# Kernel tuning notes

Hardware: AMD Instinct MI355X
Metric: run time of the kernel (lower is better)

Reference implementation:

```python
import jax, jax.numpy as jnp
import numpy as np

N_NODES = 8192
N_EDGES = 8192
DEG = 32          # nodes per hyperedge
NNZ = N_EDGES * DEG
D = 32            # embedding_dim / hidden_channels


def setup_inputs() -> dict:
    key = jax.random.key(0)
    ks = jax.random.split(key, 12)
    x_0 = jax.random.normal(ks[0], (N_NODES, D), dtype=jnp.float32)
    # incidence structure: each hyperedge touches DEG random nodes
    node_idx = jax.random.randint(ks[1], (NNZ,), 0, N_NODES)
    edge_idx = jnp.repeat(jnp.arange(N_EDGES), DEG)
    incidence_1 = jnp.zeros((N_NODES, N_EDGES), jnp.float32).at[node_idx, edge_idx].set(1.0)
    s = 1.0 / np.sqrt(D)
    # UniGCN layer weights (level-2 conv linear transform per layer, 2 layers)
    W_l1 = jax.random.uniform(ks[2], (D, D), jnp.float32, -s, s)
    W_l2 = jax.random.uniform(ks[3], (D, D), jnp.float32, -s, s)
    # 3-layer MLP (Linear(64,32), Linear(32,32), Linear(32,1)), no activations
    s2 = 1.0 / np.sqrt(2 * D)
    Wm1 = jax.random.uniform(ks[4], (2 * D, D), jnp.float32, -s2, s2)
    bm1 = jax.random.uniform(ks[5], (D,), jnp.float32, -s2, s2)
    Wm2 = jax.random.uniform(ks[6], (D, D), jnp.float32, -s, s)
    bm2 = jax.random.uniform(ks[7], (D,), jnp.float32, -s, s)
    Wm3 = jax.random.uniform(ks[8], (D, 1), jnp.float32, -s, s)
    bm3 = jax.random.uniform(ks[9], (1,), jnp.float32, -s, s)
    return {"x_0": x_0, "incidence_1": incidence_1,
            "W_l1": W_l1, "W_l2": W_l2,
            "Wm1": Wm1, "bm1": bm1, "Wm2": Wm2, "bm2": bm2,
            "Wm3": Wm3, "bm3": bm3,
            "node_idx": node_idx, "edge_idx": edge_idx}


def _unigcn(x_0, inc, W_l1, W_l2):
    # UniGCN layer: level1 (0->1, no linear transform), level2 (1->0, linear)
    x_1 = inc.T @ x_0                 # [E, D]
    x_0 = inc @ (x_1 @ W_l1)          # [N, D]
    x_1 = inc.T @ x_0                 # [E, D]
    x_0 = inc @ (x_1 @ W_l2)          # [N, D]
    return x_0, x_1


def reference(x_0, incidence_1, W_l1, W_l2, Wm1, bm1, Wm2, bm2, Wm3, bm3,
              node_idx, edge_idx):
    x_0_new, x_1_new = _unigcn(x_0, incidence_1, W_l1, W_l2)
    # gather embeddings at incidence nonzeros
    h = jnp.concatenate([x_0_new[node_idx], x_1_new[edge_idx]], axis=1)  # [NNZ, 2D]
    h = h @ Wm1 + bm1
    h = h @ Wm2 + bm2
    vals = (h @ Wm3 + bm3)[:, 0]                                          # [NNZ]
    # scatter back into dense [N, E] matrix
    output_counts = jnp.zeros_like(incidence_1).at[node_idx, edge_idx].set(vals)
    return output_counts
```

## Files before the change

### kernel.cpp

```cpp
#include <hip/hip_runtime.h>

#define N_NODES 8192
#define N_EDGES 8192
#define DEG 32
#define D 32
#define CAP 128

typedef float vf4 __attribute__((ext_vector_type(4)));


__global__ void __launch_bounds__(256)
k1_edge(const float* __restrict__ x0, const float* __restrict__ Wl1,
        const float* __restrict__ Wl2, const float* __restrict__ Wm1,
        const float* __restrict__ bm1, const float* __restrict__ Wm2,
        const float* __restrict__ bm2, const float* __restrict__ Wm3,
        const float* __restrict__ bm3, const int* __restrict__ node_idx,
        float* __restrict__ A, unsigned* __restrict__ validmask,
        int* __restrict__ cursor, int* __restrict__ csr_e,
        float* __restrict__ consts) {
    __shared__ int sidx[8][32];
    __shared__ unsigned smask[8];
    __shared__ float fsh[128];
    const int t = threadIdx.x, el = t >> 5, s = t & 31;

    if (blockIdx.x == 0) {
        float* w23 = fsh;
        float* M0  = fsh + 32;
        float* M1  = fsh + 64;
        float* w2u = fsh + 96;
        if (t < 32) {
            float acc = 0.f;
            for (int k = 0; k < 32; ++k) acc += Wm2[t * 32 + k] * Wm3[k];
            w23[t] = acc;
        }
        __syncthreads();
        if (t < 64) {
            float acc = 0.f;
            for (int k = 0; k < 32; ++k) acc += Wm1[t * 32 + k] * w23[k];
            if (t < 32) M0[t] = acc; else M1[t - 32] = acc;
        }
        if (t == 0) {
            float c = bm3[0];
            for (int k = 0; k < 32; ++k) c += bm1[k] * w23[k] + bm2[k] * Wm3[k];
            consts[0] = c;
        }
        __syncthreads();
        if (t < 32) {
            float acc = 0.f;
            for (int d2 = 0; d2 < 32; ++d2) acc += Wl2[t * 32 + d2] * M0[d2];
            w2u[t] = acc;
        }
        __syncthreads();
        if (t < 32) {
            float ay = 0.f, az = 0.f;
            for (int d2 = 0; d2 < 32; ++d2) {
                float w = Wl1[t * 32 + d2];
                ay += w * w2u[d2];
                az += w * M1[d2];
            }
            consts[1 + t]  = ay;
            consts[33 + t] = az;
        }
        __syncthreads();
    }

    int e = blockIdx.x * 8 + el;
    int idx = node_idx[e * DEG + s];
    sidx[el][s] = idx;
    __syncthreads();
    bool valid = true;
    for (int j = 0; j < s; ++j)
        if (sidx[el][j] == idx) { valid = false; break; }
    unsigned long long bl = __ballot(valid);
    if (s == 0) {
        unsigned m = (unsigned)(bl >> (t & 32));
        smask[el] = m;
        validmask[e] = m;
    }
    if (valid) {
        int pos = atomicAdd(&cursor[idx], 1);
        if (pos < CAP) csr_e[idx * CAP + pos] = e;
    }
    __syncthreads();
    unsigned m = smask[el];
    float acc = 0.f;
#pragma unroll
    for (int j = 0; j < 32; ++j)
        if ((m >> j) & 1u) acc += x0[sidx[el][j] * D + s];
    A[e * D + s] = acc;
}

__global__ void __launch_bounds__(256)
k2_node(const float* __restrict__ A, const int* __restrict__ csr_e,
        const int* __restrict__ cursor, const float* __restrict__ consts,
        float* __restrict__ y, float* __restrict__ z) {
    const int t = threadIdx.x, el = t >> 5, s = t & 31;
    int n = blockIdx.x * 8 + el;
    int cnt = min(cursor[n], CAP);
    const int* lst = csr_e + n * CAP;
    float acc = 0.f;
    int j = 0;
    for (; j + 4 <= cnt; j += 4) {
        int4 e4 = *(const int4*)(lst + j);
        acc += A[e4.x * D + s] + A[e4.y * D + s] +
               A[e4.z * D + s] + A[e4.w * D + s];
    }
    for (; j < cnt; ++j) acc += A[lst[j] * D + s];
    float ay = acc * consts[1 + s];
    float az = acc * consts[33 + s];
#pragma unroll
    for (int off = 16; off; off >>= 1) {
        ay += __shfl_xor(ay, off);
        az += __shfl_xor(az, off);
    }
    if (s == 0) { y[n] = ay; z[n] = az; }
}

__global__ void __launch_bounds__(256)
k2_edge(const int* __restrict__ node_idx, const unsigned* __restrict__ validmask,
        const float* __restrict__ y, const float* __restrict__ z,
        float* __restrict__ qw, float* __restrict__ q) {
    const int t = threadIdx.x, el = t >> 5, s = t & 31;
    int e = blockIdx.x * 8 + el;
    unsigned m = validmask[e];
    int idx = node_idx[e * DEG + s];
    bool valid = (m >> s) & 1u;
    float ay = valid ? y[idx] : 0.f;
    float az = valid ? z[idx] : 0.f;
#pragma unroll
    for (int off = 16; off; off >>= 1) {
        ay += __shfl_xor(ay, off);
        az += __shfl_xor(az, off);
    }
    if (s == 0) { qw[e] = ay; q[e] = az; }
}

__global__ void __launch_bounds__(256)
k3_out(const int* __restrict__ csr_e, const int* __restrict__ cursor,
       const float* __restrict__ qw, const float* __restrict__ q,
       const float* __restrict__ consts, float* __restrict__ out) {
    __shared__ float row[N_EDGES];
    __shared__ int eid[CAP];
    __shared__ float sp;
    const int t = threadIdx.x;
    const int n = blockIdx.x;
    const int cnt = min(cursor[n], CAP);
    if (t < CAP) eid[t] = csr_e[n * CAP + t];
    vf4* r4 = (vf4*)row;
    vf4 zz = (vf4)(0.f);
#pragma unroll
    for (int k = 0; k < 8; ++k) r4[t + 256 * k] = zz;
    __syncthreads();
    if (t < 32) {
        float v = 0.f;
        for (int j = t; j < cnt; j += 32) v += qw[eid[j]];
#pragma unroll
        for (int off = 16; off; off >>= 1) v += __shfl_xor(v, off);
        if (t == 0) sp = v + consts[0];
    }
    __syncthreads();
    float pn = sp;
    for (int j = t; j < cnt; j += 256) {
        int e = eid[j];
        row[e] = pn + q[e];
    }
    __syncthreads();
    vf4* g4 = (vf4*)(out + (size_t)n * N_EDGES);
#pragma unroll
    for (int k = 0; k < 8; ++k) g4[t + 256 * k] = r4[t + 256 * k];
}

extern "C" void kernel_launch(void* const* d_in, const int* in_sizes, int n_in,
                              void* d_out, int out_size, void* d_ws, size_t ws_size,
                              hipStream_t stream) {
    const float* x0  = (const float*)d_in[0];
    const float* Wl1 = (const float*)d_in[2];
    const float* Wl2 = (const float*)d_in[3];
    const float* Wm1 = (const float*)d_in[4];
    const float* bm1 = (const float*)d_in[5];
    const float* Wm2 = (const float*)d_in[6];
    const float* bm2 = (const float*)d_in[7];
    const float* Wm3 = (const float*)d_in[8];
    const float* bm3 = (const float*)d_in[9];
    const int* node_idx = (const int*)d_in[10];
    float* out = (float*)d_out;

    char* ws = (char*)d_ws;
    int*      cursor    = (int*)(ws);
    float*    y         = (float*)(ws + ( 32u << 10));
    float*    z         = (float*)(ws + ( 64u << 10));
    unsigned* validmask = (unsigned*)(ws + ( 96u << 10));
    float*    qw        = (float*)(ws + (128u << 10));
    float*    q         = (float*)(ws + (160u << 10));
    float*    consts    = (float*)(ws + (192u << 10));
    float*    A         = (float*)(ws + (1u << 20));
    int*      csr_e     = (int*)(ws + (2u << 20));

    hipMemsetAsync(cursor, 0, N_NODES * sizeof(int), stream);
    k1_edge<<<N_EDGES / 8, 256, 0, stream>>>(x0, Wl1, Wl2, Wm1, bm1, Wm2, bm2,
                                             Wm3, bm3, node_idx, A, validmask,
                                             cursor, csr_e, consts);
    k2_node<<<N_NODES / 8, 256, 0, stream>>>(A, csr_e, cursor, consts, y, z);
    k2_edge<<<N_EDGES / 8, 256, 0, stream>>>(node_idx, validmask, y, z, qw, q);
    k3_out<<<N_NODES, 256, 0, stream>>>(csr_e, cursor, qw, q, consts, out);
}
```

Measured before the change: 87.94 us.

## Zero-fill output in first kernel and scatter nonzeros in a sparse patch kernel

The dense 256MB output zero-fill moves out of the final per-row kernel and into the first kernel. It runs as a grid-stride store loop across 2048 blocks, with the edge-gather work done by the first 1024 of them. The final kernel now only writes the nonzero entries, one warp per node, scattering into the already-zeroed rows. The aim is to overlap the bandwidth-bound fill with the early graph work and to drop the shared-memory row staging. In exchange, the patch kernel does uncoalesced scattered stores, and the fill now sits on the critical path before the later kernels.

```diff
diff --git a/kernel.cpp b/kernel.cpp
--- a/kernel.cpp
+++ b/kernel.cpp
@@ -5,89 +5,99 @@
 #define DEG 32
 #define D 32
 #define CAP 128
+#define FILL_GRID 2048
 
 typedef float vf4 __attribute__((ext_vector_type(4)));
 
 
 __global__ void __launch_bounds__(256)
-k1_edge(const float* __restrict__ x0, const float* __restrict__ Wl1,
+k1_fill(const float* __restrict__ x0, const float* __restrict__ Wl1,
         const float* __restrict__ Wl2, const float* __restrict__ Wm1,
         const float* __restrict__ bm1, const float* __restrict__ Wm2,
         const float* __restrict__ bm2, const float* __restrict__ Wm3,
         const float* __restrict__ bm3, const int* __restrict__ node_idx,
         float* __restrict__ A, unsigned* __restrict__ validmask,
         int* __restrict__ cursor, int* __restrict__ csr_e,
-        float* __restrict__ consts) {
-    __shared__ int sidx[8][32];
-    __shared__ unsigned smask[8];
-    __shared__ float fsh[128];
-    const int t = threadIdx.x, el = t >> 5, s = t & 31;
-
-    if (blockIdx.x == 0) {
-        float* w23 = fsh;
-        float* M0  = fsh + 32;
-        float* M1  = fsh + 64;
-        float* w2u = fsh + 96;
-        if (t < 32) {
-            float acc = 0.f;
-            for (int k = 0; k < 32; ++k) acc += Wm2[t * 32 + k] * Wm3[k];
-            w23[t] = acc;
+        float* __restrict__ consts, float* __restrict__ out) {
+    const int t = threadIdx.x, el = t >> 5, s = t & 31;
+
+    if (blockIdx.x < N_EDGES / 8) {
+        __shared__ int sidx[8][32];
+        __shared__ unsigned smask[8];
+        __shared__ float fsh[128];
+        if (blockIdx.x == 0) {
+            float* w23 = fsh;
+            float* M0  = fsh + 32;
+            float* M1  = fsh + 64;
+            float* w2u = fsh + 96;
+            if (t < 32) {
+                float acc = 0.f;
+                for (int k = 0; k < 32; ++k) acc += Wm2[t * 32 + k] * Wm3[k];
+                w23[t] = acc;
+            }
+            __syncthreads();
+            if (t < 64) {
+                float acc = 0.f;
+                for (int k = 0; k < 32; ++k) acc += Wm1[t * 32 + k] * w23[k];
+                if (t < 32) M0[t] = acc; else M1[t - 32] = acc;
+            }
+            if (t == 0) {
+                float c = bm3[0];
+                for (int k = 0; k < 32; ++k) c += bm1[k] * w23[k] + bm2[k] * Wm3[k];
+                consts[0] = c;
+            }
+            __syncthreads();
+            if (t < 32) {
+                float acc = 0.f;
+                for (int d2 = 0; d2 < 32; ++d2) acc += Wl2[t * 32 + d2] * M0[d2];
+                w2u[t] = acc;
+            }
+            __syncthreads();
+            if (t < 32) {
+                float ay = 0.f, az = 0.f;
+                for (int d2 = 0; d2 < 32; ++d2) {
+                    float w = Wl1[t * 32 + d2];
+                    ay += w * w2u[d2];
+                    az += w * M1[d2];
+                }
+                consts[1 + t]  = ay;
+                consts[33 + t] = az;
+            }
+            __syncthreads();
+        }
+
+        int e = blockIdx.x * 8 + el;
+        int idx = node_idx[e * DEG + s];
+        sidx[el][s] = idx;
+        __syncthreads();
+        bool valid = true;
+        for (int j = 0; j < s; ++j)
+            if (sidx[el][j] == idx) { valid = false; break; }
+        unsigned long long bl = __ballot(valid);
+        if (s == 0) {
+            unsigned m = (unsigned)(bl >> (t & 32));
+            smask[el] = m;
+            validmask[e] = m;
+        }
+        if (valid) {
+            int pos = atomicAdd(&cursor[idx], 1);
+            if (pos < CAP) csr_e[idx * CAP + pos] = e;
         }
         __syncthreads();
-        if (t < 64) {
-            float acc = 0.f;
-            for (int k = 0; k < 32; ++k) acc += Wm1[t * 32 + k] * w23[k];
-            if (t < 32) M0[t] = acc; else M1[t - 32] = acc;
-        }
-        if (t == 0) {
-            float c = bm3[0];
-            for (int k = 0; k < 32; ++k) c += bm1[k] * w23[k] + bm2[k] * Wm3[k];
-            consts[0] = c;
-        }
-        __syncthreads();
-        if (t < 32) {
-            float acc = 0.f;
-            for (int d2 = 0; d2 < 32; ++d2) acc += Wl2[t * 32 + d2] * M0[d2];
-            w2u[t] = acc;
-        }
-        __syncthreads();
-        if (t < 32) {
-            float ay = 0.f, az = 0.f;
-            for (int d2 = 0; d2 < 32; ++d2) {
-                float w = Wl1[t * 32 + d2];
-                ay += w * w2u[d2];
-                az += w * M1[d2];
-            }
-            consts[1 + t]  = ay;
-            consts[33 + t] = az;
-        }
-        __syncthreads();
-    }
-
-    int e = blockIdx.x * 8 + el;
-    int idx = node_idx[e * DEG + s];
-    sidx[el][s] = idx;
-    __syncthreads();
-    bool valid = true;
-    for (int j = 0; j < s; ++j)
-        if (sidx[el][j] == idx) { valid = false; break; }
-    unsigned long long bl = __ballot(valid);
-    if (s == 0) {
-        unsigned m = (unsigned)(bl >> (t & 32));
-        smask[el] = m;
-        validmask[e] = m;
-    }
-    if (valid) {
-        int pos = atomicAdd(&cursor[idx], 1);
-        if (pos < CAP) csr_e[idx * CAP + pos] = e;
-    }
-    __syncthreads();
-    unsigned m = smask[el];
-    float acc = 0.f;
-#pragma unroll
-    for (int j = 0; j < 32; ++j)
-        if ((m >> j) & 1u) acc += x0[sidx[el][j] * D + s];
-    A[e * D + s] = acc;
+        unsigned m = smask[el];
+        float acc = 0.f;
+#pragma unroll
+        for (int j = 0; j < 32; ++j)
+            if ((m >> j) & 1u) acc += x0[sidx[el][j] * D + s];
+        A[e * D + s] = acc;
+    }
+
+    vf4* dst = (vf4*)out;
+    const long long nvec = (long long)N_NODES * N_EDGES / 4;
+    const long long stride = (long long)FILL_GRID * 256;
+    vf4 zz = (vf4)(0.f);
+    for (long long i = (long long)blockIdx.x * 256 + t; i < nvec; i += stride)
+        dst[i] = zz;
 }
 
 __global__ void __launch_bounds__(256)
@@ -136,38 +146,23 @@
 }
 
 __global__ void __launch_bounds__(256)
-k3_out(const int* __restrict__ csr_e, const int* __restrict__ cursor,
-       const float* __restrict__ qw, const float* __restrict__ q,
-       const float* __restrict__ consts, float* __restrict__ out) {
-    __shared__ float row[N_EDGES];
-    __shared__ int eid[CAP];
-    __shared__ float sp;
-    const int t = threadIdx.x;
-    const int n = blockIdx.x;
-    const int cnt = min(cursor[n], CAP);
-    if (t < CAP) eid[t] = csr_e[n * CAP + t];
-    vf4* r4 = (vf4*)row;
-    vf4 zz = (vf4)(0.f);
-#pragma unroll
-    for (int k = 0; k < 8; ++k) r4[t + 256 * k] = zz;
-    __syncthreads();
-    if (t < 32) {
-        float v = 0.f;
-        for (int j = t; j < cnt; j += 32) v += qw[eid[j]];
-#pragma unroll
-        for (int off = 16; off; off >>= 1) v += __shfl_xor(v, off);
-        if (t == 0) sp = v + consts[0];
-    }
-    __syncthreads();
-    float pn = sp;
-    for (int j = t; j < cnt; j += 256) {
-        int e = eid[j];
-        row[e] = pn + q[e];
-    }
-    __syncthreads();
-    vf4* g4 = (vf4*)(out + (size_t)n * N_EDGES);
-#pragma unroll
-    for (int k = 0; k < 8; ++k) g4[t + 256 * k] = r4[t + 256 * k];
+k_patch(const int* __restrict__ csr_e, const int* __restrict__ cursor,
+        const float* __restrict__ qw, const float* __restrict__ q,
+        const float* __restrict__ consts, float* __restrict__ out) {
+    const int t = threadIdx.x, el = t >> 5, s = t & 31;
+    int n = blockIdx.x * 8 + el;
+    int cnt = min(cursor[n], CAP);
+    const int* lst = csr_e + n * CAP;
+    float acc = 0.f;
+    for (int j = s; j < cnt; j += 32) acc += qw[lst[j]];
+#pragma unroll
+    for (int off = 16; off; off >>= 1) acc += __shfl_xor(acc, off);
+    float pn = acc + consts[0];
+    float* rowp = out + (size_t)n * N_EDGES;
+    for (int j = s; j < cnt; j += 32) {
+        int e = lst[j];
+        rowp[e] = pn + q[e];
+    }
 }
 
 extern "C" void kernel_launch(void* const* d_in, const int* in_sizes, int n_in,
@@ -197,10 +192,10 @@
     int*      csr_e     = (int*)(ws + (2u << 20));
 
     hipMemsetAsync(cursor, 0, N_NODES * sizeof(int), stream);
-    k1_edge<<<N_EDGES / 8, 256, 0, stream>>>(x0, Wl1, Wl2, Wm1, bm1, Wm2, bm2,
-                                             Wm3, bm3, node_idx, A, validmask,
-                                             cursor, csr_e, consts);
+    k1_fill<<<FILL_GRID, 256, 0, stream>>>(x0, Wl1, Wl2, Wm1, bm1, Wm2, bm2,
+                                           Wm3, bm3, node_idx, A, validmask,
+                                           cursor, csr_e, consts, out);
     k2_node<<<N_NODES / 8, 256, 0, stream>>>(A, csr_e, cursor, consts, y, z);
     k2_edge<<<N_EDGES / 8, 256, 0, stream>>>(node_idx, validmask, y, z, qw, q);
-    k3_out<<<N_NODES, 256, 0, stream>>>(csr_e, cursor, qw, q, consts, out);
-}
+    k_patch<<<N_NODES / 8, 256, 0, stream>>>(csr_e, cursor, qw, q, consts, out);
+}
```

Result: faster. 82.40 us (-6.3%).
